# Kernel optimization log

Measured on AMD Instinct MI355X. Metric: run time of the kernel, lower is better.

## Reference

```python
import jax, jax.numpy as jnp
import numpy as np

B, S, HID = 2, 2048, 2048
H, KVH, D = 16, 4, 128
GROUPS = H // KVH
THETA = 10000.0
SCALE = 1.0 / np.sqrt(D).astype(np.float32)
NEG = -1e9


def setup_inputs() -> dict:
    key = jax.random.key(0)
    ks = jax.random.split(key, 6)
    x = jax.random.normal(ks[0], (B, S, HID), dtype=jnp.float32)
    # causal additive mask, broadcast over heads
    causal = jnp.triu(jnp.full((S, S), NEG, dtype=jnp.float32), k=1)
    attn_mask = jnp.broadcast_to(causal, (B, 1, S, S))
    pos_ids = jnp.broadcast_to(jnp.arange(S, dtype=jnp.int32), (B, S))
    sd = 0.02
    Wq = jax.random.normal(ks[1], (H * D, HID), dtype=jnp.float32) * sd
    Wk = jax.random.normal(ks[2], (KVH * D, HID), dtype=jnp.float32) * sd
    Wv = jax.random.normal(ks[3], (KVH * D, HID), dtype=jnp.float32) * sd
    Wo = jax.random.normal(ks[4], (HID, H * D), dtype=jnp.float32) * sd
    return {"x": x, "attn_mask": attn_mask, "pos_ids": pos_ids,
            "Wq": Wq, "Wk": Wk, "Wv": Wv, "Wo": Wo}


def _rope_cos_sin(pos_ids):
    # pos_ids: [B, S] -> cos/sin: [B, 1, S, D]
    inv_freq = 1.0 / (THETA ** (jnp.arange(0, D, 2, dtype=jnp.float32) / D))
    freqs = pos_ids.astype(jnp.float32)[:, :, None] * inv_freq  # [B, S, D/2]
    emb = jnp.concatenate([freqs, freqs], axis=-1)              # [B, S, D]
    return jnp.cos(emb)[:, None], jnp.sin(emb)[:, None]


def _rotate_half(t):
    t1, t2 = jnp.split(t, 2, axis=-1)
    return jnp.concatenate([-t2, t1], axis=-1)


def reference(x, attn_mask, pos_ids, Wq, Wk, Wv, Wo):
    b, s, _ = x.shape
    q = jnp.einsum('bsh,oh->bso', x, Wq).reshape(b, s, H, D).transpose(0, 2, 1, 3)
    k = jnp.einsum('bsh,oh->bso', x, Wk).reshape(b, s, KVH, D).transpose(0, 2, 1, 3)
    v = jnp.einsum('bsh,oh->bso', x, Wv).reshape(b, s, KVH, D).transpose(0, 2, 1, 3)
    cos, sin = _rope_cos_sin(pos_ids)
    q = q * cos + _rotate_half(q) * sin
    k = k * cos + _rotate_half(k) * sin
    # GQA: repeat kv heads
    k = jnp.repeat(k, GROUPS, axis=1)  # [b, H, s, D]
    v = jnp.repeat(v, GROUPS, axis=1)
    scores = jnp.einsum('bhqd,bhkd->bhqk', q, k) * SCALE + attn_mask
    weights = jax.nn.softmax(scores, axis=-1)  # dropout p=0 (eval)
    out = jnp.einsum('bhqk,bhkd->bhqd', weights, v)
    out = out.transpose(0, 2, 1, 3).reshape(b, s, H * D)
    return jnp.einsum('bso,ho->bsh', out, Wo)
```

## Files before the change

kernel.cpp:

```cpp
#include <hip/hip_runtime.h>
#include <hip/hip_bf16.h>
#include <stdint.h>

#define B_   2
#define S_   2048
#define HID_ 2048
#define H_   16
#define KVH_ 4
#define D_   128
#define SCALE_ 0.08838834764831845f
#define QSC_ (SCALE_ * 1.4426950408889634f)

typedef __attribute__((ext_vector_type(8))) short bf16x8;
typedef __attribute__((ext_vector_type(4))) float f32x4;
typedef __attribute__((ext_vector_type(4))) short short4v;

__device__ __forceinline__ void async_copy16(void* lds, const void* g) {
  __builtin_amdgcn_global_load_lds((__attribute__((address_space(1))) void*)(uintptr_t)g,
                                   (__attribute__((address_space(3))) void*)lds, 16, 0, 0);
}

__device__ __forceinline__ short bf16bits(float f) {
  __hip_bfloat16 t = __float2bfloat16(f);
  return __builtin_bit_cast(short, t);
}
__device__ __forceinline__ float bf16tof(short s) {
  return __bfloat162float(__builtin_bit_cast(__hip_bfloat16, s));
}

__global__ __launch_bounds__(256) void f2b_all(const float4* __restrict__ x,
                                               const float4* __restrict__ wq,
                                               const float4* __restrict__ wk,
                                               const float4* __restrict__ wv,
                                               const float4* __restrict__ wo,
                                               short4v* __restrict__ xb,
                                               short4v* __restrict__ wqb,
                                               short4v* __restrict__ wkb,
                                               short4v* __restrict__ wvb,
                                               short4v* __restrict__ wob) {
  int i = blockIdx.x * blockDim.x + threadIdx.x;
  const float4* src; short4v* dst; int off;
  if (i < 2097152)      { src = x;  dst = xb;  off = 0; }
  else if (i < 3145728) { src = wq; dst = wqb; off = 2097152; }
  else if (i < 3407872) { src = wk; dst = wkb; off = 3145728; }
  else if (i < 3670016) { src = wv; dst = wvb; off = 3407872; }
  else                  { src = wo; dst = wob; off = 3670016; }
  int k = i - off;
  float4 v = src[k];
  short4v o;
  o[0] = bf16bits(v.x); o[1] = bf16bits(v.y);
  o[2] = bf16bits(v.z); o[3] = bf16bits(v.w);
  dst[k] = o;
}

template <int MODE, bool DBUF>
__global__ __launch_bounds__(256) void gemm_bt(const __hip_bfloat16* __restrict__ A,
                                               const __hip_bfloat16* __restrict__ Bw,
                                               void* __restrict__ Cout,
                                               void* __restrict__ Cout2,
                                               void* __restrict__ Cout3,
                                               int M, int N, int K) {
  __shared__ __align__(16) __hip_bfloat16 Asm[DBUF ? 2 : 1][128 * 64];
  __shared__ __align__(16) __hip_bfloat16 Bsm[DBUF ? 2 : 1][128 * 64];
  const int tid  = threadIdx.x;
  const int lane = tid & 63;
  const int wid  = tid >> 6;
  const int nwg = gridDim.x * gridDim.y;
  const int id  = blockIdx.y * gridDim.x + blockIdx.x;
  const int swz = (id & 7) * (nwg >> 3) + (id >> 3);
  const int m0 = (swz / gridDim.x) * 128;
  const int n0 = (swz % gridDim.x) * 128;
  const int qm = (wid >> 1) * 64;
  const int qn = (wid & 1) * 64;
  const int ar = lane & 15;
  const int ag = lane >> 4;
  const int srow = tid >> 3;
  const int sun  = tid & 7;

  auto STAGE = [&](int sb, int k0) {
#pragma unroll
    for (int c = 0; c < 4; ++c) {
      const int row = c * 32 + srow;
      const int cu  = sun ^ (row & 7);
      async_copy16(&Asm[sb][c * 2048 + tid * 8], A  + (size_t)(m0 + row) * K + k0 + cu * 8);
      async_copy16(&Bsm[sb][c * 2048 + tid * 8], Bw + (size_t)(n0 + row) * K + k0 + cu * 8);
    }
  };

  auto COMPUTE = [&](int sb, f32x4 (&acc)[4][4]) {
#pragma unroll
    for (int kk = 0; kk < 2; ++kk) {
      bf16x8 af[4], bfr[4];
#pragma unroll
      for (int i = 0; i < 4; ++i) {
        const int row = qm + i * 16 + ar;
        const int u = (kk * 4 + ag) ^ (row & 7);
        af[i] = *(const bf16x8*)(&Asm[sb][row * 64 + u * 8]);
      }
#pragma unroll
      for (int j = 0; j < 4; ++j) {
        const int row = qn + j * 16 + ar;
        const int u = (kk * 4 + ag) ^ (row & 7);
        bfr[j] = *(const bf16x8*)(&Bsm[sb][row * 64 + u * 8]);
      }
#pragma unroll
      for (int i = 0; i < 4; ++i)
#pragma unroll
        for (int j = 0; j < 4; ++j)
          acc[i][j] = __builtin_amdgcn_mfma_f32_16x16x32_bf16(af[i], bfr[j], acc[i][j], 0, 0, 0);
    }
  };

  f32x4 acc[4][4] = {};

  if constexpr (DBUF) {
    STAGE(0, 0);
    asm volatile("s_waitcnt vmcnt(0)" ::: "memory");
    __syncthreads();
    int cur = 0;
    for (int k0 = 0; k0 < K; k0 += 64) {
      if (k0 + 64 < K) STAGE(cur ^ 1, k0 + 64);
      COMPUTE(cur, acc);
      asm volatile("s_waitcnt vmcnt(0)" ::: "memory");
      __syncthreads();
      cur ^= 1;
    }
  } else {
    for (int k0 = 0; k0 < K; k0 += 64) {
      STAGE(0, k0);
      __syncthreads();
      COMPUTE(0, acc);
      __syncthreads();
    }
  }

  const int rb = (lane >> 4) * 4;
  const int cl = lane & 15;
#pragma unroll
  for (int i = 0; i < 4; ++i)
#pragma unroll
    for (int j = 0; j < 4; ++j) {
      const int n = n0 + qn + j * 16 + cl;
#pragma unroll
      for (int r = 0; r < 4; ++r) {
        const int m = m0 + qm + i * 16 + rb + r;
        float v = acc[i][j][r];
        if (MODE == 3) {
          ((float*)Cout)[(size_t)m * N + n] = v;
        } else {
          const int bb = m >> 11, ss = m & (S_ - 1);
          if (n < 2048) {
            const int hh = n >> 7, dd = n & 127;
            ((__hip_bfloat16*)Cout)[(((size_t)bb * 16 + hh) * S_ + ss) * D_ + dd] = __float2bfloat16(v);
          } else if (n < 2560) {
            const int n2 = n - 2048, hh = n2 >> 7, dd = n2 & 127;
            ((__hip_bfloat16*)Cout2)[(((size_t)bb * 4 + hh) * S_ + ss) * D_ + dd] = __float2bfloat16(v);
          } else {
            const int n2 = n - 2560, hh = n2 >> 7, dd = n2 & 127;
            ((__hip_bfloat16*)Cout3)[(((size_t)bb * 4 + hh) * D_ + dd) * S_ + ss] = __float2bfloat16(v);
          }
        }
      }
    }
}

__global__ __launch_bounds__(256) void rope_inplace(__hip_bfloat16* __restrict__ buf,
                                                    const int* __restrict__ pos_ids,
                                                    int lognh, float scale) {
  int idx = blockIdx.x * blockDim.x + threadIdx.x;
  int t  = idx & 15;
  int s  = (idx >> 4) & (S_ - 1);
  int bh = idx >> 15;
  int b  = bh >> lognh;
  float pos = (float)pos_ids[b * S_ + s];
  size_t base = ((size_t)bh * S_ + s) * D_ + t * 4;
  short4v lo = *(short4v*)(buf + base);
  short4v hi = *(short4v*)(buf + base + 64);
  short4v lo2, hi2;
#pragma unroll
  for (int e = 0; e < 4; ++e) {
    float d = (float)(t * 4 + e);
    float ang = pos * exp2f(d * -0.20762050593046014f);
    float c = cosf(ang), sn = sinf(ang);
    float lv = bf16tof(lo[e]), hv = bf16tof(hi[e]);
    lo2[e] = bf16bits((lv * c - hv * sn) * scale);
    hi2[e] = bf16bits((hv * c + lv * sn) * scale);
  }
  *(short4v*)(buf + base)      = lo2;
  *(short4v*)(buf + base + 64) = hi2;
}

__global__ __launch_bounds__(256, 2) void flash_attn7(const __hip_bfloat16* __restrict__ Q,
                                                      const __hip_bfloat16* __restrict__ K,
                                                      const __hip_bfloat16* __restrict__ Vt,
                                                      __hip_bfloat16* __restrict__ O) {
  __shared__ __align__(16) __hip_bfloat16 Ksm[2][64 * 128];
  __shared__ __align__(16) __hip_bfloat16 Vsm[2][128 * 64];
  __shared__ __align__(16) __hip_bfloat16 Psm[4][16 * 64];
  const int lane = threadIdx.x & 63;
  const int wid  = threadIdx.x >> 6;
  const int i   = blockIdx.x;
  const int xcd = i & 7;
  const int j   = i >> 3;
  const int bh  = xcd * 4 + (j & 3);
  const int qt  = 31 - (j >> 2);
  const int b   = bh >> 4;
  const int h   = bh & 15;
  const int kvh = h >> 2;
  const int qrow0 = qt * 64 + wid * 16;
  const int ar = lane & 15;
  const int ag = lane >> 4;
  const int q  = qrow0 + ar;
  const int nkv = qt + 1;

  const __hip_bfloat16* Qb = Q  + ((size_t)bh * S_ + qrow0) * D_;
  const __hip_bfloat16* Kb = K  + (size_t)(b * KVH_ + kvh) * S_ * D_;
  const __hip_bfloat16* Vb = Vt + (size_t)(b * KVH_ + kvh) * D_ * S_;

  bf16x8 qf[4];
#pragma unroll
  for (int kf = 0; kf < 4; ++kf)
    qf[kf] = *(const bf16x8*)(Qb + (size_t)ar * D_ + kf * 32 + ag * 8);

  auto STAGE = [&](int sb, int t) {
    const int kv0 = t * 64;
#pragma unroll
    for (int c = 0; c < 4; ++c) {
      const int idx = wid * 4 + c;
      const int rowK = idx * 4 + (lane >> 4);
      const int gcK  = (lane & 15) ^ (rowK & 7);
      async_copy16(&Ksm[sb][idx * 512 + lane * 8],
                   Kb + (size_t)(kv0 + rowK) * D_ + gcK * 8);
      const int rowV = idx * 8 + (lane >> 3);
      const int gcV  = (lane & 7) ^ (rowV & 7);
      async_copy16(&Vsm[sb][idx * 512 + lane * 8],
                   Vb + (size_t)rowV * S_ + kv0 + gcV * 8);
    }
  };

  f32x4 acc[8] = {};
  float l = 0.f;
  char* pb = (char*)&Psm[wid][0];

  STAGE(0, 0);
  asm volatile("s_waitcnt vmcnt(0)" ::: "memory");
  __syncthreads();

  int buf = 0;
  for (int t = 0; t < nkv; ++t, buf ^= 1) {
    if (t + 1 < nkv) STAGE(buf ^ 1, t + 1);
    const int kv0 = t * 64;
    f32x4 st[4] = {};
    const char* kbase = (const char*)&Ksm[buf][0];
    __builtin_amdgcn_s_setprio(1);
#pragma unroll
    for (int kvt = 0; kvt < 4; ++kvt) {
      const int rr = kvt * 16 + ar;
      const int rx = rr & 7;
#pragma unroll
      for (int kf = 0; kf < 4; ++kf) {
        const bf16x8 kfrag = *(const bf16x8*)(kbase + rr * 256 + (((kf * 4 + ag) ^ rx) << 4));
        st[kvt] = __builtin_amdgcn_mfma_f32_16x16x32_bf16(kfrag, qf[kf], st[kvt], 0, 0, 0);
      }
    }
    __builtin_amdgcn_s_setprio(0);
    const bool needmask = (t == nkv - 1);
    float psum = 0.f;
#pragma unroll
    for (int kvt = 0; kvt < 4; ++kvt) {
      short4v pk;
#pragma unroll
      for (int r = 0; r < 4; ++r) {
        float s = st[kvt][r];
        if (needmask && (kv0 + kvt * 16 + ag * 4 + r > q)) s = -3.0e38f;
        const float p = exp2f(s - 8.f);
        psum += p;
        pk[r] = bf16bits(p);
      }
      const int g = kvt * 2 + (ag >> 1);
      *(short4v*)(pb + ar * 128 + ((g ^ (ar & 7)) << 4) + (ag & 1) * 8) = pk;
    }
    psum += __shfl_xor(psum, 16, 64);
    psum += __shfl_xor(psum, 32, 64);
    l += psum;
    asm volatile("s_waitcnt lgkmcnt(0)" ::: "memory");
    const bf16x8 pf0 = *(const bf16x8*)(pb + ar * 128 + ((ag ^ (ar & 7)) << 4));
    const bf16x8 pf1 = *(const bf16x8*)(pb + ar * 128 + (((4 + ag) ^ (ar & 7)) << 4));
    const char* vbase = (const char*)&Vsm[buf][0];
    __builtin_amdgcn_s_setprio(1);
#pragma unroll
    for (int df = 0; df < 8; ++df) {
      const int rr = df * 16 + ar;
      const int rx = rr & 7;
      const bf16x8 v0 = *(const bf16x8*)(vbase + rr * 128 + ((ag ^ rx) << 4));
      const bf16x8 v1 = *(const bf16x8*)(vbase + rr * 128 + (((4 + ag) ^ rx) << 4));
      acc[df] = __builtin_amdgcn_mfma_f32_16x16x32_bf16(v0, pf0, acc[df], 0, 0, 0);
      acc[df] = __builtin_amdgcn_mfma_f32_16x16x32_bf16(v1, pf1, acc[df], 0, 0, 0);
    }
    __builtin_amdgcn_s_setprio(0);
    asm volatile("s_waitcnt vmcnt(0)" ::: "memory");
    __syncthreads();
  }

  const float linv = 1.f / l;
  __hip_bfloat16* Ob = O + ((size_t)b * S_ + qrow0 + ar) * (H_ * D_) + h * D_;
#pragma unroll
  for (int df = 0; df < 8; ++df) {
    short4v o4;
#pragma unroll
    for (int r = 0; r < 4; ++r)
      o4[r] = bf16bits(acc[df][r] * linv);
    *(short4v*)(Ob + df * 16 + ag * 4) = o4;
  }
}

extern "C" void kernel_launch(void* const* d_in, const int* in_sizes, int n_in,
                              void* d_out, int out_size, void* d_ws, size_t ws_size,
                              hipStream_t stream) {
  (void)in_sizes; (void)n_in; (void)out_size; (void)ws_size;
  const float* x  = (const float*)d_in[0];
  const int* pos  = (const int*)d_in[2];
  const float* Wq = (const float*)d_in[3];
  const float* Wk = (const float*)d_in[4];
  const float* Wv = (const float*)d_in[5];
  const float* Wo = (const float*)d_in[6];

  char* ws = (char*)d_ws;
  __hip_bfloat16* xb   = (__hip_bfloat16*)(ws);
  __hip_bfloat16* wqb  = (__hip_bfloat16*)(ws + 16777216);
  __hip_bfloat16* wkb  = (__hip_bfloat16*)(ws + 25165824);
  __hip_bfloat16* wvb  = (__hip_bfloat16*)(ws + 27262976);
  __hip_bfloat16* wob  = (__hip_bfloat16*)(ws + 29360128);
  __hip_bfloat16* qb16 = (__hip_bfloat16*)(ws + 37748736);
  __hip_bfloat16* kb16 = (__hip_bfloat16*)(ws + 54525952);
  __hip_bfloat16* vt16 = (__hip_bfloat16*)(ws + 58720256);
  __hip_bfloat16* attn = (__hip_bfloat16*)(ws + 62914560);

  f2b_all<<<18432, 256, 0, stream>>>((const float4*)x, (const float4*)Wq, (const float4*)Wk,
                                     (const float4*)Wv, (const float4*)Wo,
                                     (short4v*)xb, (short4v*)wqb, (short4v*)wkb,
                                     (short4v*)wvb, (short4v*)wob);

  gemm_bt<5, false><<<dim3(24, 32), 256, 0, stream>>>(xb, wqb, qb16, kb16, vt16, 4096, 3072, 2048);

  rope_inplace<<<4096, 256, 0, stream>>>(qb16, pos, 4, QSC_);
  rope_inplace<<<1024, 256, 0, stream>>>(kb16, pos, 2, 1.0f);

  flash_attn7<<<1024, 256, 0, stream>>>(qb16, kb16, vt16, attn);

  gemm_bt<3, true><<<dim3(16, 32), 256, 0, stream>>>(attn, wob, d_out, nullptr, nullptr, 4096, 2048, 2048);
}
```

Before: 199.4 us.

## Read V from global directly, merge rope launches, relax GEMM pipeline waits

Flash attention no longer stages V tiles through shared memory. Each lane now loads its V fragments straight from global memory, which halves LDS use and allows four blocks per CU instead of two. The two rope launches become one kernel. The GEMM double-buffer loop now waits only for the previous stage (vmcnt(8)) and uses raw barriers instead of a full drain each iteration. The risks are extra global-load latency on the PV path and a possible race on LDS visibility, since s_barrier without lgkm/vm waits depends on the vmcnt accounting being exact.

```diff
diff --git a/kernel.cpp b/kernel.cpp
--- a/kernel.cpp
+++ b/kernel.cpp
@@ -87,7 +87,9 @@
     }
   };
 
-  auto COMPUTE = [&](int sb, f32x4 (&acc)[4][4]) {
+  f32x4 acc[4][4] = {};
+
+  auto COMPUTE = [&](int sb) {
 #pragma unroll
     for (int kk = 0; kk < 2; ++kk) {
       bf16x8 af[4], bfr[4];
@@ -111,25 +113,26 @@
     }
   };
 
-  f32x4 acc[4][4] = {};
-
   if constexpr (DBUF) {
     STAGE(0, 0);
-    asm volatile("s_waitcnt vmcnt(0)" ::: "memory");
-    __syncthreads();
     int cur = 0;
     for (int k0 = 0; k0 < K; k0 += 64) {
-      if (k0 + 64 < K) STAGE(cur ^ 1, k0 + 64);
-      COMPUTE(cur, acc);
-      asm volatile("s_waitcnt vmcnt(0)" ::: "memory");
-      __syncthreads();
+      if (k0 + 64 < K) {
+        STAGE(cur ^ 1, k0 + 64);
+        asm volatile("s_waitcnt vmcnt(8)" ::: "memory");
+      } else {
+        asm volatile("s_waitcnt vmcnt(0)" ::: "memory");
+      }
+      __builtin_amdgcn_s_barrier();
+      COMPUTE(cur);
+      __builtin_amdgcn_s_barrier();
       cur ^= 1;
     }
   } else {
     for (int k0 = 0; k0 < K; k0 += 64) {
       STAGE(0, k0);
       __syncthreads();
-      COMPUTE(0, acc);
+      COMPUTE(0);
       __syncthreads();
     }
   }
@@ -164,14 +167,21 @@
     }
 }
 
-__global__ __launch_bounds__(256) void rope_inplace(__hip_bfloat16* __restrict__ buf,
-                                                    const int* __restrict__ pos_ids,
-                                                    int lognh, float scale) {
+__global__ __launch_bounds__(256) void rope_all(__hip_bfloat16* __restrict__ qb,
+                                                __hip_bfloat16* __restrict__ kb,
+                                                const int* __restrict__ pos_ids) {
   int idx = blockIdx.x * blockDim.x + threadIdx.x;
-  int t  = idx & 15;
-  int s  = (idx >> 4) & (S_ - 1);
-  int bh = idx >> 15;
-  int b  = bh >> lognh;
+  __hip_bfloat16* buf;
+  float scale;
+  int b, rel;
+  if (idx < 1048576) {
+    rel = idx; buf = qb; scale = QSC_; b = (rel >> 15) >> 4;
+  } else {
+    rel = idx - 1048576; buf = kb; scale = 1.0f; b = (rel >> 15) >> 2;
+  }
+  const int t  = rel & 15;
+  const int s  = (rel >> 4) & (S_ - 1);
+  const int bh = rel >> 15;
   float pos = (float)pos_ids[b * S_ + s];
   size_t base = ((size_t)bh * S_ + s) * D_ + t * 4;
   short4v lo = *(short4v*)(buf + base);
@@ -190,12 +200,11 @@
   *(short4v*)(buf + base + 64) = hi2;
 }
 
-__global__ __launch_bounds__(256, 2) void flash_attn7(const __hip_bfloat16* __restrict__ Q,
+__global__ __launch_bounds__(256, 4) void flash_attn8(const __hip_bfloat16* __restrict__ Q,
                                                       const __hip_bfloat16* __restrict__ K,
                                                       const __hip_bfloat16* __restrict__ Vt,
                                                       __hip_bfloat16* __restrict__ O) {
   __shared__ __align__(16) __hip_bfloat16 Ksm[2][64 * 128];
-  __shared__ __align__(16) __hip_bfloat16 Vsm[2][128 * 64];
   __shared__ __align__(16) __hip_bfloat16 Psm[4][16 * 64];
   const int lane = threadIdx.x & 63;
   const int wid  = threadIdx.x >> 6;
@@ -231,10 +240,6 @@
       const int gcK  = (lane & 15) ^ (rowK & 7);
       async_copy16(&Ksm[sb][idx * 512 + lane * 8],
                    Kb + (size_t)(kv0 + rowK) * D_ + gcK * 8);
-      const int rowV = idx * 8 + (lane >> 3);
-      const int gcV  = (lane & 7) ^ (rowV & 7);
-      async_copy16(&Vsm[sb][idx * 512 + lane * 8],
-                   Vb + (size_t)rowV * S_ + kv0 + gcV * 8);
     }
   };
 
@@ -286,14 +291,12 @@
     asm volatile("s_waitcnt lgkmcnt(0)" ::: "memory");
     const bf16x8 pf0 = *(const bf16x8*)(pb + ar * 128 + ((ag ^ (ar & 7)) << 4));
     const bf16x8 pf1 = *(const bf16x8*)(pb + ar * 128 + (((4 + ag) ^ (ar & 7)) << 4));
-    const char* vbase = (const char*)&Vsm[buf][0];
     __builtin_amdgcn_s_setprio(1);
 #pragma unroll
     for (int df = 0; df < 8; ++df) {
-      const int rr = df * 16 + ar;
-      const int rx = rr & 7;
-      const bf16x8 v0 = *(const bf16x8*)(vbase + rr * 128 + ((ag ^ rx) << 4));
-      const bf16x8 v1 = *(const bf16x8*)(vbase + rr * 128 + (((4 + ag) ^ rx) << 4));
+      const __hip_bfloat16* vp = Vb + (size_t)(df * 16 + ar) * S_ + kv0 + ag * 8;
+      const bf16x8 v0 = *(const bf16x8*)(vp);
+      const bf16x8 v1 = *(const bf16x8*)(vp + 32);
       acc[df] = __builtin_amdgcn_mfma_f32_16x16x32_bf16(v0, pf0, acc[df], 0, 0, 0);
       acc[df] = __builtin_amdgcn_mfma_f32_16x16x32_bf16(v1, pf1, acc[df], 0, 0, 0);
     }
@@ -343,10 +346,9 @@
 
   gemm_bt<5, false><<<dim3(24, 32), 256, 0, stream>>>(xb, wqb, qb16, kb16, vt16, 4096, 3072, 2048);
 
-  rope_inplace<<<4096, 256, 0, stream>>>(qb16, pos, 4, QSC_);
-  rope_inplace<<<1024, 256, 0, stream>>>(kb16, pos, 2, 1.0f);
-
-  flash_attn7<<<1024, 256, 0, stream>>>(qb16, kb16, vt16, attn);
+  rope_all<<<5120, 256, 0, stream>>>(qb16, kb16, pos);
+
+  flash_attn8<<<1024, 256, 0, stream>>>(qb16, kb16, vt16, attn);
 
   gemm_bt<3, true><<<dim3(16, 32), 256, 0, stream>>>(attn, wob, d_out, nullptr, nullptr, 4096, 2048, 2048);
 }
```

Result: slower. 303.1 us (+52.0%).
